# Kernel tuning notes

Measured on AMD Instinct MI355X. Metric: run time of the kernel, lower is better.

The kernel has to match this reference:

```python
import jax, jax.numpy as jnp
import numpy as np

N = 50000      # nodes
E = 800000     # edges per metapath
M = 3          # metapaths
H = 2          # heads
IN = 128       # in_dim
HID = 64       # hidden
HEAD = HID // H
OUT = 16       # classes
ATT = 128      # atten_dim


def setup_inputs() -> dict:
    key = jax.random.key(0)
    ks = jax.random.split(key, 12)
    s = 0.05
    return {
        "x": jax.random.normal(ks[0], (N, IN), jnp.float32),
        "edge_index": jax.random.randint(ks[1], (M, 2, E), 0, N, dtype=jnp.int64),
        # per-(metapath, head) GCN params
        "W_enc": jax.random.normal(ks[2], (M, H, IN, HID), jnp.float32) * s,
        "b_enc": jnp.zeros((M, H, HID), jnp.float32),
        "W_conv": jax.random.normal(ks[3], (M, H, HID, HID), jnp.float32) * s,
        "b_conv": jnp.zeros((M, H, HID), jnp.float32),
        "W_dec": jax.random.normal(ks[4], (M, H, HID, HEAD), jnp.float32) * s,
        "b_dec": jnp.zeros((M, H, HEAD), jnp.float32),
        # semantic attention params
        "W_s": jax.random.normal(ks[5], (HID, ATT), jnp.float32) * s,
        "b_s": jnp.zeros((ATT,), jnp.float32),
        "q": jax.random.normal(ks[6], (ATT,), jnp.float32) * s,
        # output projection
        "W_o": jax.random.normal(ks[7], (HID, OUT), jnp.float32) * s,
        "b_o": jnp.zeros((OUT,), jnp.float32),
    }


def _lrelu(v, slope=0.1):
    return jnp.where(v > 0, v, slope * v)


def reference(x, edge_index, W_enc, b_enc, W_conv, b_conv, W_dec, b_dec, W_s, b_s, q, W_o, b_o):
    # encoder for all (metapath, head) at once: [M,H,N,HID]
    h = _lrelu(jnp.einsum('ni,mhio->mhno', x, W_enc) + b_enc[:, :, None, :])

    z_list = []
    for m in range(M):  # small fixed number of metapaths
        src = edge_index[m, 0]
        dst = edge_index[m, 1]
        # GCNConv with self-loops + symmetric normalization (PyG semantics)
        deg = jax.ops.segment_sum(jnp.ones(E, jnp.float32), dst, num_segments=N) + 1.0
        inv_sqrt = jax.lax.rsqrt(deg)
        coef = inv_sqrt[src] * inv_sqrt[dst]                 # [E]
        xw = jnp.einsum('hnd,hdo->hno', h[m], W_conv[m])     # [H,N,HID]
        msg = xw[:, src, :] * coef[None, :, None]            # [H,E,HID] gather
        agg = jax.vmap(lambda mm: jax.ops.segment_sum(mm, dst, num_segments=N))(msg)
        agg = agg + xw * (1.0 / deg)[None, :, None]          # self-loop term (norm = 1/deg)
        agg = agg + b_conv[m][:, None, :]
        hh = _lrelu(agg)
        dec = jnp.einsum('hnd,hdo->hno', hh, W_dec[m]) + b_dec[m][:, None, :]  # [H,N,HEAD]
        z_list.append(jnp.transpose(dec, (1, 0, 2)).reshape(N, HID))           # head concat

    zs = jnp.stack(z_list)                                   # [M,N,HID]
    # semantic attention over metapaths
    hs = jnp.tanh(jnp.einsum('mnd,da->mna', zs, W_s) + b_s)
    beta = jax.nn.softmax(jnp.einsum('mna,a->mn', hs, q).mean(axis=1))  # [M]
    Z = jnp.einsum('m,mnd->nd', beta, zs)                    # [N,HID]
    out = jax.nn.log_softmax(Z @ W_o + b_o, axis=-1)         # [N,OUT]
    return out, beta
```

## Files before the change

kernel.cpp:

```cpp
#include <hip/hip_runtime.h>

#define NN 50000
#define EE 800000
#define MM 3
#define HH 2
#define IND 128
#define HIDD 64
#define HEADD 32
#define OUTD 16
#define ATTD 128

#define NBKT 64
#define BSZ 782

#define NG4 200000
#define BBLK 196
#define QCAP 13200

#define GLS 136
#define XWN 50048
#define PN  50048

typedef unsigned char u8;
typedef unsigned short u16;
typedef unsigned long long u64;
typedef short bf16x8 __attribute__((ext_vector_type(8)));
typedef unsigned short u16x8 __attribute__((ext_vector_type(8)));
typedef u64 u64x2 __attribute__((ext_vector_type(2)));
typedef unsigned int u32x4 __attribute__((ext_vector_type(4)));
typedef float f32x2 __attribute__((ext_vector_type(2)));
typedef float f32x4 __attribute__((ext_vector_type(4)));

__device__ __forceinline__ float lrelu(float v) { return v > 0.f ? v : 0.1f * v; }

__device__ __forceinline__ float fast_tanh(float x) {
    float ax = fabsf(x);
    float e = __expf(-2.0f * ax);
    float t = (1.0f - e) * __builtin_amdgcn_rcpf(1.0f + e);
    return copysignf(t, x);
}

__device__ __forceinline__ u16 f2b(float f) {
    union { float f; unsigned int u; } v; v.f = f;
    unsigned int r = v.u + 0x7fffu + ((v.u >> 16) & 1u);
    return (u16)(r >> 16);
}
__device__ __forceinline__ float b2f(u16 u) {
    union { unsigned int u; float f; } v; v.u = ((unsigned int)u) << 16; return v.f;
}

__device__ __forceinline__ u8 f2e4hw(float f) {
    int r = __builtin_amdgcn_cvt_pk_fp8_f32(f, f, 0, false);
    return (u8)(r & 0xff);
}

__device__ __forceinline__ void acc16(f32x2* acc, u32x4 w) {
#pragma unroll
    for (int i = 0; i < 4; i++) {
        acc[2 * i]     += __builtin_amdgcn_cvt_pk_f32_fp8(w[i], false);
        acc[2 * i + 1] += __builtin_amdgcn_cvt_pk_f32_fp8(w[i], true);
    }
}

__global__ __launch_bounds__(256) void k_bucket(const int* __restrict__ ei,
                                                u64* __restrict__ queues,
                                                int* __restrict__ gcur) {
    __shared__ int cnt[NBKT];
    __shared__ int base[NBKT];
    const int m = blockIdx.y, tid = threadIdx.x;
    const int4* s4 = (const int4*)(ei + (size_t)m * 2 * EE);
    const int4* d4 = (const int4*)(ei + (size_t)m * 2 * EE + EE);
    const int q0 = blockIdx.x * 1024;
    if (tid < NBKT) cnt[tid] = 0;
    __syncthreads();
#pragma unroll
    for (int i = 0; i < 4; i++) {
        int q = q0 + i * 256 + tid;
        if (q < NG4) {
            int4 v = d4[q];
            atomicAdd(&cnt[v.x / BSZ], 1);
            atomicAdd(&cnt[v.y / BSZ], 1);
            atomicAdd(&cnt[v.z / BSZ], 1);
            atomicAdd(&cnt[v.w / BSZ], 1);
        }
    }
    __syncthreads();
    if (tid < NBKT) { base[tid] = atomicAdd(&gcur[m * NBKT + tid], cnt[tid]); cnt[tid] = 0; }
    __syncthreads();
#pragma unroll
    for (int i = 0; i < 4; i++) {
        int q = q0 + i * 256 + tid;
        if (q < NG4) {
            int4 dv = d4[q];
            int4 sv = s4[q];
            int ds[4] = {dv.x, dv.y, dv.z, dv.w};
            int ss[4] = {sv.x, sv.y, sv.z, sv.w};
#pragma unroll
            for (int e = 0; e < 4; e++) {
                int b = ds[e] / BSZ;
                int slot = base[b] + atomicAdd(&cnt[b], 1);
                if (slot < QCAP) {
                    u64 pk = ((u64)(unsigned)ds[e] << 32) | (unsigned)ss[e];
                    queues[((size_t)(m * NBKT + b)) * QCAP + slot] = pk;
                }
            }
        }
    }
}

__global__ void k_pscan(const int* __restrict__ gcur, int* __restrict__ pbase) {
    int t = threadIdx.x;
    if (t < MM) {
        int run = 0;
        for (int b = 0; b < NBKT; b++) {
            int L = gcur[t * NBKT + b]; if (L > QCAP) L = QCAP;
            pbase[t * NBKT + b] = run; run += L;
        }
    }
}

__global__ __launch_bounds__(512) void k_csr(const u64* __restrict__ queues,
                                             const int* __restrict__ gcur,
                                             const int* __restrict__ pbase,
                                             int* __restrict__ ofs,
                                             float* __restrict__ rs,
                                             int* __restrict__ sorted) {
    __shared__ int cnt[BSZ];
    __shared__ int wscan[8];
    const int m = blockIdx.y;
    const int b = blockIdx.x;
    const int tid = threadIdx.x;
    const int lane = tid & 63, w = tid >> 6;
    int qlen = gcur[m * NBKT + b]; if (qlen > QCAP) qlen = QCAP;
    const u64* q = queues + ((size_t)(m * NBKT + b)) * QCAP;
    const u64x2* q2 = (const u64x2*)q;
    const int dlo = b * BSZ;
    const int nd = min(dlo + BSZ, NN) - dlo;
    const int n2 = qlen >> 1;
    for (int i = tid; i < BSZ; i += 512) cnt[i] = 0;
    __syncthreads();
    for (int i = tid; i < n2; i += 512) {
        u64x2 e = q2[i];
        atomicAdd(&cnt[(int)(e.x >> 32) - dlo], 1);
        atomicAdd(&cnt[(int)(e.y >> 32) - dlo], 1);
    }
    if (tid == 0 && (qlen & 1))
        atomicAdd(&cnt[(int)(q[qlen - 1] >> 32) - dlo], 1);
    __syncthreads();
    const int c0 = tid * 2;
    int v0 = (c0 < BSZ) ? cnt[c0] : 0;
    int v1 = (c0 + 1 < BSZ) ? cnt[c0 + 1] : 0;
    int s = v0 + v1;
    int vv = s;
    for (int off = 1; off < 64; off <<= 1) { int t = __shfl_up(vv, off); if (lane >= off) vv += t; }
    if (lane == 63) wscan[w] = vv;
    __syncthreads();
    if (tid == 0) { int run = 0; for (int j = 0; j < 8; j++) { int t = wscan[j]; wscan[j] = run; run += t; } }
    __syncthreads();
    int excl = wscan[w] + vv - s;
    int g0 = pbase[m * NBKT + b] + excl;
    int g1 = g0 + v0;
    if (c0 < nd) {
        ofs[(size_t)m * (NN + 1) + dlo + c0] = g0;
        rs[(size_t)m * NN + dlo + c0] = rsqrtf((float)(v0 + 1));
    }
    if (c0 + 1 < nd) {
        ofs[(size_t)m * (NN + 1) + dlo + c0 + 1] = g1;
        rs[(size_t)m * NN + dlo + c0 + 1] = rsqrtf((float)(v1 + 1));
    }
    if (b == NBKT - 1 && tid == 0)
        ofs[(size_t)m * (NN + 1) + NN] = EE;
    __syncthreads();
    if (c0 < BSZ) cnt[c0] = g0;
    if (c0 + 1 < BSZ) cnt[c0 + 1] = g1;
    __syncthreads();
    int* srt = sorted + (size_t)m * EE;
    for (int i = tid; i < n2; i += 512) {
        u64x2 e = q2[i];
        int p0 = atomicAdd(&cnt[(int)(e.x >> 32) - dlo], 1);
        srt[p0] = (int)(e.x & 0xffffffffu);
        int p1 = atomicAdd(&cnt[(int)(e.y >> 32) - dlo], 1);
        srt[p1] = (int)(e.y & 0xffffffffu);
    }
    if (tid == 0 && (qlen & 1)) {
        u64 e = q[qlen - 1];
        int p0 = atomicAdd(&cnt[(int)(e >> 32) - dlo], 1);
        srt[p0] = (int)(e & 0xffffffffu);
    }
}

__global__ __launch_bounds__(256) void k_perm(const int* __restrict__ ofs_all,
                                              int* __restrict__ perm_all) {
    __shared__ int dl[256];
    const int m = blockIdx.y;
    const int t = threadIdx.x;
    const int sub = t >> 6, li = t & 63;
    const int base = blockIdx.x * 256 + sub * 64;
    const int* ofs = ofs_all + (size_t)m * (NN + 1);
    const int g = base + li;
    int d = (g < NN) ? (ofs[g + 1] - ofs[g]) : -1;
    dl[t] = d;
    __syncthreads();
    if (base < PN) {
        const int* dls = &dl[sub * 64];
        int rank = 0;
        for (int j = 0; j < 64; j++) {
            int dj = dls[j];
            rank += (dj > d || (dj == d && j < li)) ? 1 : 0;
        }
        perm_all[(size_t)m * PN + base + rank] = li;
    }
}

__global__ __launch_bounds__(256) void k_prep(const float* __restrict__ We, const float* __restrict__ Wc,
                                              const float* __restrict__ Wd, const float* __restrict__ Ws,
                                              u16* __restrict__ wbe, u16* __restrict__ wbc,
                                              u16* __restrict__ wbd, u16* __restrict__ wbs) {
    int t = blockIdx.x * 256 + threadIdx.x;
    if (t >= 11776) return;
    bf16x8 val;
    u16* dst;
    if (t < 6144) {
        int m = t >> 11, r = t & 2047;
        int nt = r >> 8, ks = (r >> 6) & 3, lane = r & 63;
        int n = nt * 16 + (lane & 15), h = n >> 6, o = n & 63;
        int kb = ks * 32 + (lane >> 4) * 8;
        const float* w = We + ((size_t)(m * 2 + h) * 128) * 64;
#pragma unroll
        for (int j = 0; j < 8; j++) val[j] = (short)f2b(w[(size_t)(kb + j) * 64 + o]);
        dst = wbe + ((size_t)m * 2048 + r) * 8;
    } else if (t < 9216) {
        int u = t - 6144;
        int m = u >> 10, r = u & 1023;
        int nt = r >> 7, ks = (r >> 6) & 1, lane = r & 63;
        int h = nt >> 2, o = (nt & 3) * 16 + (lane & 15);
        int kb = ks * 32 + (lane >> 4) * 8;
        const float* w = Wc + ((size_t)(m * 2 + h) * 64) * 64;
#pragma unroll
        for (int j = 0; j < 8; j++) val[j] = (short)f2b(w[(size_t)(kb + j) * 64 + o]);
        dst = wbc + ((size_t)m * 1024 + r) * 8;
    } else if (t < 10752) {
        int u = t - 9216;
        int m = u >> 9, r = u & 511;
        int nt = r >> 7, ks = (r >> 6) & 1, lane = r & 63;
        int h = nt >> 1, o = (nt & 1) * 16 + (lane & 15);
        int kb = ks * 32 + (lane >> 4) * 8;
        const float* w = Wd + ((size_t)(m * 2 + h) * 64) * 32;
#pragma unroll
        for (int j = 0; j < 8; j++) val[j] = (short)f2b(w[(size_t)(kb + j) * 32 + o]);
        dst = wbd + ((size_t)m * 512 + r) * 8;
    } else {
        int r = t - 10752;
        int nt = r >> 7, ks = (r >> 6) & 1, lane = r & 63;
        int n = nt * 16 + (lane & 15);
        int kb = ks * 32 + (lane >> 4) * 8;
#pragma unroll
        for (int j = 0; j < 8; j++) val[j] = (short)f2b(Ws[(size_t)(kb + j) * 128 + n]);
        dst = wbs + (size_t)r * 8;
    }
    *(bf16x8*)dst = val;
}

#define HLS 133
__global__ __launch_bounds__(256) void k_encconv(const float* __restrict__ x,
                                                 const u16* __restrict__ wbe_all,
                                                 const float* __restrict__ be_all,
                                                 const u16* __restrict__ wbc_all,
                                                 const float* __restrict__ rs_all,
                                                 u8* __restrict__ xw_all) {
    __shared__ float hl[64 * HLS];
    const int tid = threadIdx.x, lane = tid & 63, wave = tid >> 6;
    const int quad = lane >> 4, c16 = lane & 15;
    const int row = blockIdx.x * 64 + wave * 16 + c16;
    const bool ok = row < NN;
    const int rbl = wave * 16 + quad * 4;
    const int rl = wave * 16 + c16;
    f32x4 zero = {0.f, 0.f, 0.f, 0.f};

    bf16x8 a[4];
#pragma unroll
    for (int ks = 0; ks < 4; ks++) {
        bf16x8 t = {0, 0, 0, 0, 0, 0, 0, 0};
        if (ok) {
            const float* xp = x + (size_t)row * 128 + ks * 32 + quad * 8;
            float4 xa = *(const float4*)xp;
            float4 xb = *(const float4*)(xp + 4);
            t[0] = (short)f2b(xa.x); t[1] = (short)f2b(xa.y);
            t[2] = (short)f2b(xa.z); t[3] = (short)f2b(xa.w);
            t[4] = (short)f2b(xb.x); t[5] = (short)f2b(xb.y);
            t[6] = (short)f2b(xb.z); t[7] = (short)f2b(xb.w);
        }
        a[ks] = t;
    }

    for (int m = 0; m < MM; m++) {
        const bf16x8* wbE = (const bf16x8*)(wbe_all + (size_t)m * 2048 * 8);
        const float* be = be_all + m * 2 * 64;
        const float* rs = rs_all + (size_t)m * NN;
        u8* xw = xw_all + (size_t)m * XWN * 128;

        f32x4 acc[8];
#pragma unroll
        for (int nt = 0; nt < 8; nt++) acc[nt] = zero;
#pragma unroll
        for (int ks = 0; ks < 4; ks++) {
#pragma unroll
            for (int nt = 0; nt < 8; nt++)
                acc[nt] = __builtin_amdgcn_mfma_f32_16x16x32_bf16(a[ks], wbE[(nt * 4 + ks) * 64 + lane], acc[nt], 0, 0, 0);
        }
#pragma unroll
        for (int nt = 0; nt < 8; nt++) {
            int col = nt * 16 + c16, hh = col >> 6, o = col & 63;
            float bias = be[hh * 64 + o];
#pragma unroll
            for (int j = 0; j < 4; j++) {
                int rlw = rbl + j;
                int rg = blockIdx.x * 64 + rlw;
                hl[rlw * HLS + col] = (rg < NN) ? lrelu(acc[nt][j] + bias) : 0.f;
            }
        }
        __syncthreads();
        const bf16x8* wbC = (const bf16x8*)(wbc_all + (size_t)m * 1024 * 8);
        f32x4 cacc[8];
#pragma unroll
        for (int nt = 0; nt < 8; nt++) cacc[nt] = zero;
#pragma unroll
        for (int ks = 0; ks < 2; ks++) {
            bf16x8 a0, a1;
            const float* hp = &hl[rl * HLS + ks * 32 + quad * 8];
#pragma unroll
            for (int j = 0; j < 8; j++) { a0[j] = (short)f2b(hp[j]); a1[j] = (short)f2b(hp[64 + j]); }
#pragma unroll
            for (int nt = 0; nt < 8; nt++)
                cacc[nt] = __builtin_amdgcn_mfma_f32_16x16x32_bf16(nt < 4 ? a0 : a1, wbC[(nt * 2 + ks) * 64 + lane], cacc[nt], 0, 0, 0);
        }
        float rsv[4];
#pragma unroll
        for (int j = 0; j < 4; j++) {
            int r = blockIdx.x * 64 + rbl + j;
            rsv[j] = (r < NN) ? rs[r] * 64.f : 0.f;
        }
#pragma unroll
        for (int nt = 0; nt < 8; nt++) {
            int col = nt * 16 + c16;
#pragma unroll
            for (int j = 0; j < 4; j++) {
                int r = blockIdx.x * 64 + rbl + j;
                xw[(size_t)r * 128 + col] = f2e4hw(cacc[nt][j] * rsv[j]);
            }
        }
        if (m < MM - 1) __syncthreads();
    }
}

__global__ __launch_bounds__(512) void k_gpost(const int* __restrict__ sorted_all,
                                               const int* __restrict__ ofs_all,
                                               const int* __restrict__ perm_all,
                                               const float* __restrict__ rs_all,
                                               const u8* __restrict__ xw_all,
                                               const float* __restrict__ bconv_all,
                                               const u16* __restrict__ wbd_all,
                                               const float* __restrict__ bdec_all,
                                               const u16* __restrict__ wbs,
                                               const float* __restrict__ bs,
                                               const float* __restrict__ qv,
                                               u16* __restrict__ z_all,
                                               float* __restrict__ score) {
    __shared__ u16 shm[64 * GLS];
    __shared__ float spart[8];
    u16* ggl = shm;
    float* zl = (float*)shm;
    const int m = blockIdx.y;
    const int tid = threadIdx.x, lane = tid & 63, wave = tid >> 6;
    const int* sorted = sorted_all + (size_t)m * EE;
    const int* ofs = ofs_all + (size_t)m * (NN + 1);
    const int* perm = perm_all + (size_t)m * PN;
    const float* rs = rs_all + (size_t)m * NN;
    const u8* xw = xw_all + (size_t)m * XWN * 128;
    const float* bconv = bconv_all + m * 2 * 64;
    const float* bdec = bdec_all + m * 2 * 32;
    u16* z = z_all + (size_t)m * NN * 64;

    {
        const int g = lane >> 3, c = lane & 7;
        const int pl = perm[blockIdx.x * 64 + wave * 8 + g];
        const int dst = blockIdx.x * 64 + pl;
        const bool on = dst < NN;
        int beg = 0, deg = 0;
        if (on) { beg = ofs[dst]; deg = ofs[dst + 1] - beg; }
        int degmax = max(deg, __shfl_xor(deg, 8));
        degmax = max(degmax, __shfl_xor(degmax, 16));
        degmax = max(degmax, __shfl_xor(degmax, 32));
        const int coff = c * 16;

        auto lidx = [&](int j) -> int {
            int t = j + (c & 3);
            return (t < deg) ? sorted[beg + t] : NN;
        };
        auto lrow = [&](int iv, u32x4* wv) {
#pragma unroll
            for (int k = 0; k < 4; k++) {
                int s = __shfl(iv, (lane & 0x38) + k);
                wv[k] = *(const u32x4*)&xw[(size_t)(unsigned)s * 128 + coff];
            }
        };

        f32x2 acc[8];
#pragma unroll
        for (int i = 0; i < 8; i++) acc[i] = 0.f;

        int i0 = lidx(0);
        int i1 = lidx(4);
        {
            int sd = on ? dst : NN;
            u32x4 w = *(const u32x4*)&xw[(size_t)sd * 128 + coff];
            acc16(acc, w);
        }
        u32x4 wA[4], wB[4];
        lrow(i0, wA);
        const int nch = ((degmax + 7) >> 3) * 2;
        for (int ch = 0; ch < nch; ch += 2) {
            lrow(i1, wB);
            i0 = lidx(ch * 4 + 8);
#pragma unroll
            for (int k = 0; k < 4; k++) acc16(acc, wA[k]);
            lrow(i0, wA);
            i1 = lidx(ch * 4 + 12);
#pragma unroll
            for (int k = 0; k < 4; k++) acc16(acc, wB[k]);
        }

        float rsv = on ? rs[dst] * (1.f / 64.f) : 0.f;
        u16x8 o0, o1;
#pragma unroll
        for (int i = 0; i < 4; i++) {
            o0[2 * i]     = f2b(acc[i].x * rsv);
            o0[2 * i + 1] = f2b(acc[i].y * rsv);
            o1[2 * i]     = f2b(acc[i + 4].x * rsv);
            o1[2 * i + 1] = f2b(acc[i + 4].y * rsv);
        }
        u16* gp = &ggl[pl * GLS + coff];
        *(u16x8*)gp = o0;
        *(u16x8*)(gp + 8) = o1;
    }
    __syncthreads();

    f32x4 zero = {0.f, 0.f, 0.f, 0.f};
    const int quad = lane >> 4, c16 = lane & 15;
    const int wq = wave & 3, hi = wave >> 2;
    const int rl = wq * 16 + c16;
    const bf16x8* wd = (const bf16x8*)(wbd_all + (size_t)m * 512 * 8);
    f32x4 pacc[2];
    pacc[0] = zero; pacc[1] = zero;
#pragma unroll
    for (int ks = 0; ks < 2; ks++) {
        bf16x8 a;
        int k0 = ks * 32 + quad * 8;
        u16x8 gv = *(const u16x8*)&ggl[rl * GLS + hi * 64 + k0];
#pragma unroll
        for (int j = 0; j < 8; j++)
            a[j] = (short)f2b(lrelu(b2f(gv[j]) + bconv[hi * 64 + k0 + j]));
#pragma unroll
        for (int nt2 = 0; nt2 < 2; nt2++) {
            int nt = hi * 2 + nt2;
            pacc[nt2] = __builtin_amdgcn_mfma_f32_16x16x32_bf16(a, wd[(nt * 2 + ks) * 64 + lane], pacc[nt2], 0, 0, 0);
        }
    }
    __syncthreads();
    {
        const int rbl = wq * 16 + quad * 4;
#pragma unroll
        for (int nt2 = 0; nt2 < 2; nt2++) {
            int nt = hi * 2 + nt2;
            int col = nt * 16 + c16, hh = col >> 5, o = col & 31;
            float bias = bdec[hh * 32 + o];
#pragma unroll
            for (int j = 0; j < 4; j++) {
                int rl2 = rbl + j;
                int rg = blockIdx.x * 64 + rl2;
                zl[rl2 * 68 + col] = (rg < NN) ? (pacc[nt2][j] + bias) : 0.f;
            }
        }
    }
    __syncthreads();

    {
        int rl2 = tid >> 3, cq = tid & 7;
        int rg = blockIdx.x * 64 + rl2;
        if (rg < NN) {
#pragma unroll
            for (int i = 0; i < 2; i++) {
                int c4 = (cq * 2 + i) * 4;
                float4 zv = *(const float4*)&zl[rl2 * 68 + c4];
                ushort4 o;
                o.x = f2b(zv.x); o.y = f2b(zv.y); o.z = f2b(zv.z); o.w = f2b(zv.w);
                *(ushort4*)&z[(size_t)rg * 64 + c4] = o;
            }
        }
    }
    float s = 0.f;
    {
        const bf16x8* wsb = (const bf16x8*)wbs;
        f32x4 sa[4];
#pragma unroll
        for (int nt2 = 0; nt2 < 4; nt2++) sa[nt2] = zero;
#pragma unroll
        for (int ks = 0; ks < 2; ks++) {
            bf16x8 a;
            const float* zp = &zl[rl * 68 + ks * 32 + quad * 8];
            f32x4 z0 = *(const f32x4*)zp;
            f32x4 z1 = *(const f32x4*)(zp + 4);
            a[0] = (short)f2b(z0[0]); a[1] = (short)f2b(z0[1]);
            a[2] = (short)f2b(z0[2]); a[3] = (short)f2b(z0[3]);
            a[4] = (short)f2b(z1[0]); a[5] = (short)f2b(z1[1]);
            a[6] = (short)f2b(z1[2]); a[7] = (short)f2b(z1[3]);
#pragma unroll
            for (int nt2 = 0; nt2 < 4; nt2++) {
                int nt = hi * 4 + nt2;
                sa[nt2] = __builtin_amdgcn_mfma_f32_16x16x32_bf16(a, wsb[(nt * 2 + ks) * 64 + lane], sa[nt2], 0, 0, 0);
            }
        }
        const int rbl = wq * 16 + quad * 4;
#pragma unroll
        for (int nt2 = 0; nt2 < 4; nt2++) {
            int nt = hi * 4 + nt2;
            int col = nt * 16 + c16;
            float qc = qv[col], bb = bs[col];
#pragma unroll
            for (int j = 0; j < 4; j++) {
                int rg = blockIdx.x * 64 + rbl + j;
                if (rg < NN) s += fast_tanh(sa[nt2][j] + bb) * qc;
            }
        }
#pragma unroll
        for (int off = 1; off < 64; off <<= 1) s += __shfl_xor(s, off);
    }
    if (lane == 0) spart[wave] = s;
    __syncthreads();
    if (tid == 0) {
        float t = spart[0] + spart[1] + spart[2] + spart[3]
                + spart[4] + spart[5] + spart[6] + spart[7];
        atomicAdd(&score[m], t);
    }
}

__global__ void k_beta(const float* __restrict__ score, float* __restrict__ beta_ws,
                       float* __restrict__ out) {
    if (threadIdx.x == 0) {
        float s0 = score[0] / (float)NN, s1 = score[1] / (float)NN, s2 = score[2] / (float)NN;
        float mx = fmaxf(s0, fmaxf(s1, s2));
        float e0 = expf(s0 - mx), e1 = expf(s1 - mx), e2 = expf(s2 - mx);
        float inv = 1.f / (e0 + e1 + e2);
        beta_ws[0] = e0 * inv; beta_ws[1] = e1 * inv; beta_ws[2] = e2 * inv;
        out[800000] = e0 * inv; out[800001] = e1 * inv; out[800002] = e2 * inv;
    }
}

__global__ __launch_bounds__(256) void k_out(const u16* __restrict__ z,
                                             const float* __restrict__ beta,
                                             const float* __restrict__ Wo,
                                             const float* __restrict__ bo,
                                             float* __restrict__ out) {
    __shared__ float Zt[64 * 68];
    __shared__ float Wl[64 * 16];
    __shared__ float bl[16];
    const int tid = threadIdx.x, nbase = blockIdx.x * 64;
    float b0 = beta[0], b1 = beta[1], b2 = beta[2];
    for (int qq = tid; qq < 64 * 16; qq += 256) {
        int node = qq >> 4, k4 = qq & 15;
        int ng = nbase + node;
        float4 v = make_float4(0.f, 0.f, 0.f, 0.f);
        if (ng < NN) {
            ushort4 z0 = *(const ushort4*)&z[((size_t)0 * NN + ng) * 64 + k4 * 4];
            ushort4 z1 = *(const ushort4*)&z[((size_t)1 * NN + ng) * 64 + k4 * 4];
            ushort4 z2 = *(const ushort4*)&z[((size_t)2 * NN + ng) * 64 + k4 * 4];
            v.x = b0 * b2f(z0.x) + b1 * b2f(z1.x) + b2 * b2f(z2.x);
            v.y = b0 * b2f(z0.y) + b1 * b2f(z1.y) + b2 * b2f(z2.y);
            v.z = b0 * b2f(z0.z) + b1 * b2f(z1.z) + b2 * b2f(z2.z);
            v.w = b0 * b2f(z0.w) + b1 * b2f(z1.w) + b2 * b2f(z2.w);
        }
        *(float4*)&Zt[node * 68 + k4 * 4] = v;
    }
    for (int qq = tid; qq < 64 * 16 / 4; qq += 256)
        ((float4*)Wl)[qq] = ((const float4*)Wo)[qq];
    if (tid < 16) bl[tid] = bo[tid];
    __syncthreads();

    const int node = tid >> 2, cg = tid & 3;
    float4 a = make_float4(bl[cg * 4 + 0], bl[cg * 4 + 1], bl[cg * 4 + 2], bl[cg * 4 + 3]);
    for (int k = 0; k < 64; k++) {
        float zv = Zt[node * 68 + k];
        float4 w = *(const float4*)&Wl[k * 16 + cg * 4];
        a.x = fmaf(zv, w.x, a.x);
        a.y = fmaf(zv, w.y, a.y);
        a.z = fmaf(zv, w.z, a.z);
        a.w = fmaf(zv, w.w, a.w);
    }
    float mx = fmaxf(fmaxf(a.x, a.y), fmaxf(a.z, a.w));
    mx = fmaxf(mx, __shfl_xor(mx, 1));
    mx = fmaxf(mx, __shfl_xor(mx, 2));
    float sm = expf(a.x - mx) + expf(a.y - mx) + expf(a.z - mx) + expf(a.w - mx);
    sm += __shfl_xor(sm, 1);
    sm += __shfl_xor(sm, 2);
    float lse = mx + logf(sm);
    int ng = nbase + node;
    if (ng < NN) {
        float4 r = make_float4(a.x - lse, a.y - lse, a.z - lse, a.w - lse);
        *(float4*)&out[(size_t)ng * 16 + cg * 4] = r;
    }
}

extern "C" void kernel_launch(void* const* d_in, const int* in_sizes, int n_in,
                              void* d_out, int out_size, void* d_ws, size_t ws_size,
                              hipStream_t stream) {
    const float* x      = (const float*)d_in[0];
    const int*   ei     = (const int*)d_in[1];
    const float* W_enc  = (const float*)d_in[2];
    const float* b_enc  = (const float*)d_in[3];
    const float* W_conv = (const float*)d_in[4];
    const float* b_conv = (const float*)d_in[5];
    const float* W_dec  = (const float*)d_in[6];
    const float* b_dec  = (const float*)d_in[7];
    const float* W_s    = (const float*)d_in[8];
    const float* b_s    = (const float*)d_in[9];
    const float* qv     = (const float*)d_in[10];
    const float* W_o    = (const float*)d_in[11];
    const float* b_o    = (const float*)d_in[12];
    float* out = (float*)d_out;

    char* ws = (char*)d_ws;
    size_t off = 0;
    auto alloc = [&](size_t bytes) -> char* {
        char* p = ws + off;
        off = (off + bytes + 255) & ~(size_t)255;
        return p;
    };
    int*   row_ofs = (int*)alloc((size_t)MM * (NN + 1) * 4);
    float* rs      = (float*)alloc((size_t)MM * NN * 4);
    int*   sorted  = (int*)alloc((size_t)MM * EE * 4);
    u64*   queues  = (u64*)alloc((size_t)MM * NBKT * QCAP * 8);
    int*   gcur    = (int*)alloc((size_t)MM * NBKT * 4);
    int*   pbase   = (int*)alloc((size_t)MM * NBKT * 4);
    float* score   = (float*)alloc(64);
    float* beta_ws = (float*)alloc(64);
    u16*   wbe     = (u16*)alloc((size_t)MM * 2048 * 8 * 2);
    u16*   wbc     = (u16*)alloc((size_t)MM * 1024 * 8 * 2);
    u16*   wbd     = (u16*)alloc((size_t)MM * 512 * 8 * 2);
    u16*   wbs     = (u16*)alloc((size_t)1024 * 8 * 2);
    u8*    xw_buf  = (u8*)alloc((size_t)MM * XWN * 128);
    u16*   z_buf   = (u16*)alloc((size_t)MM * NN * 64 * 2);
    int*   perm    = (int*)alloc((size_t)MM * PN * 4);

    hipMemsetAsync(gcur, 0, (size_t)MM * NBKT * 4, stream);
    hipMemsetAsync(score, 0, 16, stream);

    dim3 gbkt(BBLK, MM);
    dim3 gcsr(NBKT, MM);
    k_bucket<<<gbkt, 256, 0, stream>>>(ei, queues, gcur);
    k_pscan<<<1, 64, 0, stream>>>(gcur, pbase);
    k_csr<<<gcsr, 512, 0, stream>>>(queues, gcur, pbase, row_ofs, rs, sorted);
    k_prep<<<46, 256, 0, stream>>>(W_enc, W_conv, W_dec, W_s, wbe, wbc, wbd, wbs);

    const int GB = (NN + 63) / 64;
    dim3 gperm((GB + 3) / 4, MM);
    k_perm<<<gperm, 256, 0, stream>>>(row_ofs, perm);

    k_encconv<<<GB, 256, 0, stream>>>(x, wbe, b_enc, wbc, rs, xw_buf);
    dim3 gmm(GB, MM);
    k_gpost<<<gmm, 512, 0, stream>>>(sorted, row_ofs, perm, rs, xw_buf,
                                     b_conv, wbd, b_dec, wbs, b_s, qv,
                                     z_buf, score);
    k_beta<<<1, 64, 0, stream>>>(score, beta_ws, out);
    k_out<<<GB, 256, 0, stream>>>(z_buf, beta_ws, W_o, b_o, out);
}
```

Baseline: 266.3 us.

## Split encoder-conv across metapaths in grid and load gather indices directly per lane

The encoder+conv kernel now launches one block per (row tile, metapath) instead of looping over the three metapaths inside each block. This triples the block count for better occupancy, at the cost of re-reading x three times. Separately, the gather kernel drops the cross-lane shuffle of neighbor indices: each lane loads its four indices straight from the sorted array. That removes shuffle latency from the dependency chain but issues redundant index loads across lanes.

```diff
diff --git a/kernel.cpp b/kernel.cpp
--- a/kernel.cpp
+++ b/kernel.cpp
@@ -269,87 +269,77 @@
                                                  const float* __restrict__ rs_all,
                                                  u8* __restrict__ xw_all) {
     __shared__ float hl[64 * HLS];
+    const int m = blockIdx.y;
     const int tid = threadIdx.x, lane = tid & 63, wave = tid >> 6;
     const int quad = lane >> 4, c16 = lane & 15;
     const int row = blockIdx.x * 64 + wave * 16 + c16;
     const bool ok = row < NN;
-    const int rbl = wave * 16 + quad * 4;
-    const int rl = wave * 16 + c16;
+    const bf16x8* wbE = (const bf16x8*)(wbe_all + (size_t)m * 2048 * 8);
+    const float* be = be_all + m * 2 * 64;
+    const float* rs = rs_all + (size_t)m * NN;
+    u8* xw = xw_all + (size_t)m * XWN * 128;
     f32x4 zero = {0.f, 0.f, 0.f, 0.f};
-
-    bf16x8 a[4];
+    f32x4 acc[8];
+#pragma unroll
+    for (int nt = 0; nt < 8; nt++) acc[nt] = zero;
 #pragma unroll
     for (int ks = 0; ks < 4; ks++) {
-        bf16x8 t = {0, 0, 0, 0, 0, 0, 0, 0};
+        bf16x8 a = {0, 0, 0, 0, 0, 0, 0, 0};
         if (ok) {
             const float* xp = x + (size_t)row * 128 + ks * 32 + quad * 8;
             float4 xa = *(const float4*)xp;
             float4 xb = *(const float4*)(xp + 4);
-            t[0] = (short)f2b(xa.x); t[1] = (short)f2b(xa.y);
-            t[2] = (short)f2b(xa.z); t[3] = (short)f2b(xa.w);
-            t[4] = (short)f2b(xb.x); t[5] = (short)f2b(xb.y);
-            t[6] = (short)f2b(xb.z); t[7] = (short)f2b(xb.w);
-        }
-        a[ks] = t;
-    }
-
-    for (int m = 0; m < MM; m++) {
-        const bf16x8* wbE = (const bf16x8*)(wbe_all + (size_t)m * 2048 * 8);
-        const float* be = be_all + m * 2 * 64;
-        const float* rs = rs_all + (size_t)m * NN;
-        u8* xw = xw_all + (size_t)m * XWN * 128;
-
-        f32x4 acc[8];
-#pragma unroll
-        for (int nt = 0; nt < 8; nt++) acc[nt] = zero;
-#pragma unroll
-        for (int ks = 0; ks < 4; ks++) {
-#pragma unroll
-            for (int nt = 0; nt < 8; nt++)
-                acc[nt] = __builtin_amdgcn_mfma_f32_16x16x32_bf16(a[ks], wbE[(nt * 4 + ks) * 64 + lane], acc[nt], 0, 0, 0);
-        }
-#pragma unroll
-        for (int nt = 0; nt < 8; nt++) {
-            int col = nt * 16 + c16, hh = col >> 6, o = col & 63;
-            float bias = be[hh * 64 + o];
-#pragma unroll
-            for (int j = 0; j < 4; j++) {
-                int rlw = rbl + j;
-                int rg = blockIdx.x * 64 + rlw;
-                hl[rlw * HLS + col] = (rg < NN) ? lrelu(acc[nt][j] + bias) : 0.f;
-            }
-        }
-        __syncthreads();
-        const bf16x8* wbC = (const bf16x8*)(wbc_all + (size_t)m * 1024 * 8);
-        f32x4 cacc[8];
-#pragma unroll
-        for (int nt = 0; nt < 8; nt++) cacc[nt] = zero;
-#pragma unroll
-        for (int ks = 0; ks < 2; ks++) {
-            bf16x8 a0, a1;
-            const float* hp = &hl[rl * HLS + ks * 32 + quad * 8];
-#pragma unroll
-            for (int j = 0; j < 8; j++) { a0[j] = (short)f2b(hp[j]); a1[j] = (short)f2b(hp[64 + j]); }
-#pragma unroll
-            for (int nt = 0; nt < 8; nt++)
-                cacc[nt] = __builtin_amdgcn_mfma_f32_16x16x32_bf16(nt < 4 ? a0 : a1, wbC[(nt * 2 + ks) * 64 + lane], cacc[nt], 0, 0, 0);
-        }
-        float rsv[4];
+            a[0] = (short)f2b(xa.x); a[1] = (short)f2b(xa.y);
+            a[2] = (short)f2b(xa.z); a[3] = (short)f2b(xa.w);
+            a[4] = (short)f2b(xb.x); a[5] = (short)f2b(xb.y);
+            a[6] = (short)f2b(xb.z); a[7] = (short)f2b(xb.w);
+        }
+#pragma unroll
+        for (int nt = 0; nt < 8; nt++)
+            acc[nt] = __builtin_amdgcn_mfma_f32_16x16x32_bf16(a, wbE[(nt * 4 + ks) * 64 + lane], acc[nt], 0, 0, 0);
+    }
+    const int rbl = wave * 16 + quad * 4;
+#pragma unroll
+    for (int nt = 0; nt < 8; nt++) {
+        int col = nt * 16 + c16, hh = col >> 6, o = col & 63;
+        float bias = be[hh * 64 + o];
+#pragma unroll
+        for (int j = 0; j < 4; j++) {
+            int rl = rbl + j;
+            int rg = blockIdx.x * 64 + rl;
+            hl[rl * HLS + col] = (rg < NN) ? lrelu(acc[nt][j] + bias) : 0.f;
+        }
+    }
+    __syncthreads();
+    const bf16x8* wbC = (const bf16x8*)(wbc_all + (size_t)m * 1024 * 8);
+    f32x4 cacc[8];
+#pragma unroll
+    for (int nt = 0; nt < 8; nt++) cacc[nt] = zero;
+    const int rl = wave * 16 + c16;
+#pragma unroll
+    for (int ks = 0; ks < 2; ks++) {
+        bf16x8 a0, a1;
+        const float* hp = &hl[rl * HLS + ks * 32 + quad * 8];
+#pragma unroll
+        for (int j = 0; j < 8; j++) { a0[j] = (short)f2b(hp[j]); a1[j] = (short)f2b(hp[64 + j]); }
+#pragma unroll
+        for (int nt = 0; nt < 8; nt++)
+            cacc[nt] = __builtin_amdgcn_mfma_f32_16x16x32_bf16(nt < 4 ? a0 : a1, wbC[(nt * 2 + ks) * 64 + lane], cacc[nt], 0, 0, 0);
+    }
+    float rsv[4];
+#pragma unroll
+    for (int j = 0; j < 4; j++) {
+        int r = blockIdx.x * 64 + rbl + j;
+        rsv[j] = (r < NN) ? rs[r] * 64.f : 0.f;
+    }
+#pragma unroll
+    for (int nt = 0; nt < 8; nt++) {
+        int col = nt * 16 + c16;
 #pragma unroll
         for (int j = 0; j < 4; j++) {
             int r = blockIdx.x * 64 + rbl + j;
-            rsv[j] = (r < NN) ? rs[r] * 64.f : 0.f;
-        }
-#pragma unroll
-        for (int nt = 0; nt < 8; nt++) {
-            int col = nt * 16 + c16;
-#pragma unroll
-            for (int j = 0; j < 4; j++) {
-                int r = blockIdx.x * 64 + rbl + j;
-                xw[(size_t)r * 128 + col] = f2e4hw(cacc[nt][j] * rsv[j]);
-            }
-        }
-        if (m < MM - 1) __syncthreads();
+            xw[(size_t)r * 128 + col] = f2e4hw(cacc[nt][j] * rsv[j]);
+        }
     }
 }
 
@@ -393,39 +383,41 @@
         degmax = max(degmax, __shfl_xor(degmax, 32));
         const int coff = c * 16;
 
-        auto lidx = [&](int j) -> int {
-            int t = j + (c & 3);
-            return (t < deg) ? sorted[beg + t] : NN;
-        };
-        auto lrow = [&](int iv, u32x4* wv) {
+        auto lidx = [&](int j, int* iv) {
 #pragma unroll
             for (int k = 0; k < 4; k++) {
-                int s = __shfl(iv, (lane & 0x38) + k);
-                wv[k] = *(const u32x4*)&xw[(size_t)(unsigned)s * 128 + coff];
+                int t = j + k;
+                iv[k] = (t < deg) ? sorted[beg + t] : NN;
             }
         };
+        auto lrow = [&](const int* iv, u32x4* wv) {
+#pragma unroll
+            for (int k = 0; k < 4; k++)
+                wv[k] = *(const u32x4*)&xw[(size_t)(unsigned)iv[k] * 128 + coff];
+        };
 
         f32x2 acc[8];
 #pragma unroll
         for (int i = 0; i < 8; i++) acc[i] = 0.f;
 
-        int i0 = lidx(0);
-        int i1 = lidx(4);
+        int ivA[4], ivB[4];
+        lidx(0, ivA);
+        lidx(4, ivB);
         {
             int sd = on ? dst : NN;
             u32x4 w = *(const u32x4*)&xw[(size_t)sd * 128 + coff];
             acc16(acc, w);
         }
         u32x4 wA[4], wB[4];
-        lrow(i0, wA);
+        lrow(ivA, wA);
         const int nch = ((degmax + 7) >> 3) * 2;
         for (int ch = 0; ch < nch; ch += 2) {
-            lrow(i1, wB);
-            i0 = lidx(ch * 4 + 8);
+            lrow(ivB, wB);
+            lidx(ch * 4 + 8, ivA);
 #pragma unroll
             for (int k = 0; k < 4; k++) acc16(acc, wA[k]);
-            lrow(i0, wA);
-            i1 = lidx(ch * 4 + 12);
+            lrow(ivA, wA);
+            lidx(ch * 4 + 12, ivB);
 #pragma unroll
             for (int k = 0; k < 4; k++) acc16(acc, wB[k]);
         }
@@ -665,8 +657,8 @@
     dim3 gperm((GB + 3) / 4, MM);
     k_perm<<<gperm, 256, 0, stream>>>(row_ofs, perm);
 
-    k_encconv<<<GB, 256, 0, stream>>>(x, wbe, b_enc, wbc, rs, xw_buf);
     dim3 gmm(GB, MM);
+    k_encconv<<<gmm, 256, 0, stream>>>(x, wbe, b_enc, wbc, rs, xw_buf);
     k_gpost<<<gmm, 512, 0, stream>>>(sorted, row_ofs, perm, rs, xw_buf,
                                      b_conv, wbd, b_dec, wbs, b_s, qv,
                                      z_buf, score);
```

New measurement: 259.9 us. 2.4% less time.
